# Kernel tuning notes

Hardware: AMD Instinct MI355X
Metric: run time of the kernel (lower is better)

The kernel has to match this reference:

```python
import jax, jax.numpy as jnp
import numpy as np

NUM_INSTANCES = 64  # instance ids in [0, 64); id 0 is background and excluded


def _variance_smooth_loss(variances, ins_labels, num_segments):
    # variances: [N, D] float, ins_labels: [N] int
    N, D = variances.shape
    ones = jnp.ones((N,), dtype=variances.dtype)
    counts = jax.ops.segment_sum(ones, ins_labels, num_segments=num_segments)          # [S]
    sums = jax.ops.segment_sum(variances, ins_labels, num_segments=num_segments)       # [S, D]
    safe_counts = jnp.maximum(counts, 1.0)
    means = sums / safe_counts[:, None]                                                # per-instance mean [S, D]
    diff = variances - means[ins_labels]                                               # gather means back [N, D]
    sq = jnp.sum(diff * diff, axis=1)                                                  # [N]
    # per-instance MSE = sum of squared diffs / (K_i * D), matching nn.MSELoss (mean reduction)
    per_ins = jax.ops.segment_sum(sq, ins_labels, num_segments=num_segments) / (safe_counts * D)
    valid = (counts > 0) & (jnp.arange(num_segments) != 0)                             # skip id 0 & absent ids
    return jnp.sum(jnp.where(valid, per_ins, jnp.zeros_like(per_ins)))


def setup_inputs() -> dict:
    key = jax.random.key(0)
    k1, k2 = jax.random.split(key)
    N, D = 4_000_000, 8
    variances = jax.random.normal(k1, (N, D), dtype=jnp.float32)
    ins_labels = jax.random.randint(k2, (N,), 0, NUM_INSTANCES, dtype=jnp.int32)
    return {"variances": variances, "ins_labels": ins_labels}


def reference(variances, ins_labels):
    return _variance_smooth_loss(variances, ins_labels, NUM_INSTANCES)
```

## Files before the change

### kernel.cpp

```cpp
#include <hip/hip_runtime.h>

#define NUM_INST 64
#define BLOCK 256
#define NWAVES 4
#define GRID 2048

typedef float f32x4 __attribute__((ext_vector_type(4)));
typedef short s16x8 __attribute__((ext_vector_type(8)));
typedef int   i32x4 __attribute__((ext_vector_type(4)));

union FragU { i32x4 i; s16x8 s; };

__device__ __forceinline__ unsigned hilo_pack(float v) {
    unsigned h, p;
    asm("v_cvt_pk_bf16_f32 %0, %1, %1" : "=v"(h) : "v"(v));
    const float r = v - __uint_as_float(h << 16);
    asm("v_cvt_pk_bf16_f32 %0, %1, %2" : "=v"(p) : "v"(v), "v"(r));
    return p;
}

__global__ __launch_bounds__(BLOCK) void vsl_main(const float* __restrict__ rows,
                                                  const int* __restrict__ labels,
                                                  float* __restrict__ gacc, int n) {
    const int tid = threadIdx.x;
    const int w = tid >> 6;
    const int lane = tid & 63;
    const int g = lane >> 4;
    const int c = lane & 15;
    const int cc = c & 7;

    f32x4 accS[4], accQ[4];
#pragma unroll
    for (int t = 0; t < 4; ++t) { accS[t] = (f32x4){0,0,0,0}; accQ[t] = (f32x4){0,0,0,0}; }

    const int waveId = blockIdx.x * NWAVES + w;
    const int nWavesTot = GRID * NWAVES;
    const int nChunks = (n + 15) >> 4;

    for (int ch = waveId; ch < nChunks; ch += nWavesTot) {
        const int base = ch << 4;
        const int r0 = base + 2 * g;
        unsigned b1[4], b2[4];
        int lbl[4];

        if (base + 16 <= n) {
            const int2 lp = *(const int2*)(labels + r0);
            const int2 lq = *(const int2*)(labels + r0 + 8);
            lbl[0] = lp.x; lbl[1] = lp.y; lbl[2] = lq.x; lbl[3] = lq.y;
            const float v0 = rows[(r0    ) * 8 + cc];
            const float v1 = rows[(r0 + 1) * 8 + cc];
            const float v2 = rows[(r0 + 8) * 8 + cc];
            const float v3 = rows[(r0 + 9) * 8 + cc];
            if (c < 8) {
                b1[0] = hilo_pack(v0);      b1[1] = hilo_pack(v1);
                b1[2] = hilo_pack(v2);      b1[3] = hilo_pack(v3);
                b2[0] = hilo_pack(v0 * v0); b2[1] = hilo_pack(v1 * v1);
                b2[2] = hilo_pack(v2 * v2); b2[3] = hilo_pack(v3 * v3);
            } else {
                const unsigned one = (c == 8) ? 0x3F80u : 0u;
                b1[0] = b1[1] = b1[2] = b1[3] = one;
                b2[0] = b2[1] = b2[2] = b2[3] = 0u;
            }
        } else {
#pragma unroll
            for (int q = 0; q < 4; ++q) {
                const int rq = r0 + (q & 1) + ((q >> 1) * 8);
                const bool ok = rq < n;
                const int sq = ok ? rq : 0;
                const float vq = rows[sq * 8 + cc];
                lbl[q] = ok ? labels[sq] : -1;
                if (c < 8) {
                    b1[q] = ok ? hilo_pack(vq) : 0u;
                    b2[q] = ok ? hilo_pack(vq * vq) : 0u;
                } else {
                    b1[q] = (c == 8 && ok) ? 0x3F80u : 0u;
                    b2[q] = 0u;
                }
            }
        }

        FragU B1, B2;
        B1.i = (i32x4){(int)b1[0], (int)b1[1], (int)b1[2], (int)b1[3]};
        B2.i = (i32x4){(int)b2[0], (int)b2[1], (int)b2[2], (int)b2[3]};

#pragma unroll
        for (int t = 0; t < 4; ++t) {
            const int m = c + 16 * t;
            FragU A;
            A.i = (i32x4){ lbl[0] == m ? (int)0x3F803F80 : 0,
                           lbl[1] == m ? (int)0x3F803F80 : 0,
                           lbl[2] == m ? (int)0x3F803F80 : 0,
                           lbl[3] == m ? (int)0x3F803F80 : 0 };
            accS[t] = __builtin_amdgcn_mfma_f32_16x16x32_bf16(A.s, B1.s, accS[t], 0, 0, 0);
            accQ[t] = __builtin_amdgcn_mfma_f32_16x16x32_bf16(A.s, B2.s, accQ[t], 0, 0, 0);
        }
    }

    __shared__ float red[NWAVES][NUM_INST][12];
#pragma unroll
    for (int t = 0; t < 4; ++t) {
#pragma unroll
        for (int rg = 0; rg < 4; ++rg) {
            const int Lr = 16 * t + 4 * g + rg;
            const float vS = accS[t][rg];
            if (c < 10) red[w][Lr][(c < 8) ? c : (c == 8 ? 9 : 11)] = vS;
            float sq = accQ[t][rg];
            sq += __shfl_xor(sq, 1, 64);
            sq += __shfl_xor(sq, 2, 64);
            sq += __shfl_xor(sq, 4, 64);
            if (c == 0) red[w][Lr][8] = sq;
        }
    }
    __syncthreads();

    for (int j = tid; j < NUM_INST * 10; j += BLOCK) {
        const int Lb = j / 10;
        const int st = j - Lb * 10;
        float v = 0;
#pragma unroll
        for (int ww = 0; ww < NWAVES; ++ww) v += red[ww][Lb][st];
        atomicAdd(&gacc[j], v);
    }
}

__global__ __launch_bounds__(64) void vsl_final(const float* __restrict__ gacc,
                                                float* __restrict__ out) {
    const int s = threadIdx.x;
    float val = 0.0f;
    const float* base = &gacc[s * 10];
    const float cnt = base[9];
    if (s != 0 && cnt > 0.0f) {
        const float ss = base[8];
        float m2 = 0.0f;
#pragma unroll
        for (int d = 0; d < 8; ++d) {
            const float sd = base[d];
            m2 += sd * sd;
        }
        val = (ss - m2 / cnt) / (cnt * 8.0f);
    }
#pragma unroll
    for (int off = 32; off > 0; off >>= 1) val += __shfl_down(val, off, 64);
    if (s == 0) out[0] = val;
}

extern "C" void kernel_launch(void* const* d_in, const int* in_sizes, int n_in,
                              void* d_out, int out_size, void* d_ws, size_t ws_size,
                              hipStream_t stream) {
    const float* variances = (const float*)d_in[0];
    const int* labels = (const int*)d_in[1];
    const int n = in_sizes[1];
    float* gacc = (float*)d_ws;

    hipMemsetAsync(d_ws, 0, NUM_INST * 10 * sizeof(float), stream);
    vsl_main<<<GRID, BLOCK, 0, stream>>>(variances, labels, gacc, n);
    vsl_final<<<1, 64, 0, stream>>>(gacc, (float*)d_out);
}
```

Baseline: 241.3 us.

## Stage 64-row superchunks through LDS with register prefetch of next chunk

```diff
diff --git a/kernel.cpp b/kernel.cpp
--- a/kernel.cpp
+++ b/kernel.cpp
@@ -19,9 +19,37 @@
     return p;
 }
 
+__device__ __forceinline__ void chunk_mfma(const int* lbl, float v0, float v1,
+                                           float v2, float v3, int c,
+                                           f32x4* accS, f32x4* accQ) {
+    FragU B1, B2;
+    if (c < 8) {
+        B1.i = (i32x4){(int)hilo_pack(v0), (int)hilo_pack(v1),
+                       (int)hilo_pack(v2), (int)hilo_pack(v3)};
+        B2.i = (i32x4){(int)hilo_pack(v0 * v0), (int)hilo_pack(v1 * v1),
+                       (int)hilo_pack(v2 * v2), (int)hilo_pack(v3 * v3)};
+    } else {
+        const int one = (c == 8) ? 0x3F80 : 0;
+        B1.i = (i32x4){one, one, one, one};
+        B2.i = (i32x4){0, 0, 0, 0};
+    }
+#pragma unroll
+    for (int t = 0; t < 4; ++t) {
+        const int m = c + 16 * t;
+        FragU A;
+        A.i = (i32x4){ lbl[0] == m ? (int)0x3F803F80 : 0,
+                       lbl[1] == m ? (int)0x3F803F80 : 0,
+                       lbl[2] == m ? (int)0x3F803F80 : 0,
+                       lbl[3] == m ? (int)0x3F803F80 : 0 };
+        accS[t] = __builtin_amdgcn_mfma_f32_16x16x32_bf16(A.s, B1.s, accS[t], 0, 0, 0);
+        accQ[t] = __builtin_amdgcn_mfma_f32_16x16x32_bf16(A.s, B2.s, accQ[t], 0, 0, 0);
+    }
+}
+
 __global__ __launch_bounds__(BLOCK) void vsl_main(const float* __restrict__ rows,
                                                   const int* __restrict__ labels,
                                                   float* __restrict__ gacc, int n) {
+    __shared__ float sm[3072];
     const int tid = threadIdx.x;
     const int w = tid >> 6;
     const int lane = tid & 63;
@@ -29,86 +57,96 @@
     const int c = lane & 15;
     const int cc = c & 7;
 
+    float* const wrow = sm + w * 576;
+    int* const wlab = (int*)(wrow + 512);
+
     f32x4 accS[4], accQ[4];
 #pragma unroll
     for (int t = 0; t < 4; ++t) { accS[t] = (f32x4){0,0,0,0}; accQ[t] = (f32x4){0,0,0,0}; }
 
     const int waveId = blockIdx.x * NWAVES + w;
-    const int nWavesTot = GRID * NWAVES;
-    const int nChunks = (n + 15) >> 4;
+    const int step = GRID * NWAVES;
+    const int nSC = (n + 63) >> 6;
+    const int nFullSC = n >> 6;
 
-    for (int ch = waveId; ch < nChunks; ch += nWavesTot) {
-        const int base = ch << 4;
-        const int r0 = base + 2 * g;
-        unsigned b1[4], b2[4];
-        int lbl[4];
+    f32x4 pr0 = {0,0,0,0}, pr1 = {0,0,0,0};
+    int pl = 0;
+    int sc = waveId;
+    bool stCur = (sc < nFullSC);
+    if (stCur) {
+        const float* src = rows + (size_t)sc * 512;
+        pr0 = *(const f32x4*)(src + lane * 4);
+        pr1 = *(const f32x4*)(src + 256 + lane * 4);
+        pl = labels[sc * 64 + lane];
+    }
 
-        if (base + 16 <= n) {
-            const int2 lp = *(const int2*)(labels + r0);
-            const int2 lq = *(const int2*)(labels + r0 + 8);
-            lbl[0] = lp.x; lbl[1] = lp.y; lbl[2] = lq.x; lbl[3] = lq.y;
-            const float v0 = rows[(r0    ) * 8 + cc];
-            const float v1 = rows[(r0 + 1) * 8 + cc];
-            const float v2 = rows[(r0 + 8) * 8 + cc];
-            const float v3 = rows[(r0 + 9) * 8 + cc];
-            if (c < 8) {
-                b1[0] = hilo_pack(v0);      b1[1] = hilo_pack(v1);
-                b1[2] = hilo_pack(v2);      b1[3] = hilo_pack(v3);
-                b2[0] = hilo_pack(v0 * v0); b2[1] = hilo_pack(v1 * v1);
-                b2[2] = hilo_pack(v2 * v2); b2[3] = hilo_pack(v3 * v3);
-            } else {
-                const unsigned one = (c == 8) ? 0x3F80u : 0u;
-                b1[0] = b1[1] = b1[2] = b1[3] = one;
-                b2[0] = b2[1] = b2[2] = b2[3] = 0u;
+    for (; sc < nSC; sc += step) {
+        const int scn = sc + step;
+        const bool stNext = (scn < nFullSC);
+
+        if (stCur) {
+            *(f32x4*)(wrow + lane * 4) = pr0;
+            *(f32x4*)(wrow + 256 + lane * 4) = pr1;
+            wlab[lane] = pl;
+        }
+        f32x4 nr0 = {0,0,0,0}, nr1 = {0,0,0,0};
+        int nl = 0;
+        if (stNext) {
+            const float* src = rows + (size_t)scn * 512;
+            nr0 = *(const f32x4*)(src + lane * 4);
+            nr1 = *(const f32x4*)(src + 256 + lane * 4);
+            nl = labels[scn * 64 + lane];
+        }
+
+        if (stCur) {
+#pragma unroll
+            for (int ck = 0; ck < 4; ++ck) {
+                const float* rc = wrow + ck * 128;
+                const int* lc = wlab + ck * 16;
+                const int2 lp = *(const int2*)(lc + 2 * g);
+                const int2 lq = *(const int2*)(lc + 2 * g + 8);
+                const int lbl[4] = {lp.x, lp.y, lq.x, lq.y};
+                const float v0 = rc[g * 16 + cc];
+                const float v1 = rc[g * 16 + 8 + cc];
+                const float v2 = rc[g * 16 + 64 + cc];
+                const float v3 = rc[g * 16 + 72 + cc];
+                chunk_mfma(lbl, v0, v1, v2, v3, c, accS, accQ);
             }
         } else {
+            const int base = sc << 6;
 #pragma unroll
-            for (int q = 0; q < 4; ++q) {
-                const int rq = r0 + (q & 1) + ((q >> 1) * 8);
-                const bool ok = rq < n;
-                const int sq = ok ? rq : 0;
-                const float vq = rows[sq * 8 + cc];
-                lbl[q] = ok ? labels[sq] : -1;
-                if (c < 8) {
-                    b1[q] = ok ? hilo_pack(vq) : 0u;
-                    b2[q] = ok ? hilo_pack(vq * vq) : 0u;
-                } else {
-                    b1[q] = (c == 8 && ok) ? 0x3F80u : 0u;
-                    b2[q] = 0u;
+            for (int ck = 0; ck < 4; ++ck) {
+                const int r0 = base + ck * 16 + 2 * g;
+                int lbl[4];
+                float v[4];
+#pragma unroll
+                for (int q = 0; q < 4; ++q) {
+                    const int rq = r0 + (q & 1) + ((q >> 1) << 3);
+                    const bool ok = rq < n;
+                    const int rs = ok ? rq : 0;
+                    v[q] = rows[(size_t)rs * 8 + cc];
+                    lbl[q] = ok ? labels[rs] : -1;
                 }
+                chunk_mfma(lbl, v[0], v[1], v[2], v[3], c, accS, accQ);
             }
         }
-
-        FragU B1, B2;
-        B1.i = (i32x4){(int)b1[0], (int)b1[1], (int)b1[2], (int)b1[3]};
-        B2.i = (i32x4){(int)b2[0], (int)b2[1], (int)b2[2], (int)b2[3]};
-
-#pragma unroll
-        for (int t = 0; t < 4; ++t) {
-            const int m = c + 16 * t;
-            FragU A;
-            A.i = (i32x4){ lbl[0] == m ? (int)0x3F803F80 : 0,
-                           lbl[1] == m ? (int)0x3F803F80 : 0,
-                           lbl[2] == m ? (int)0x3F803F80 : 0,
-                           lbl[3] == m ? (int)0x3F803F80 : 0 };
-            accS[t] = __builtin_amdgcn_mfma_f32_16x16x32_bf16(A.s, B1.s, accS[t], 0, 0, 0);
-            accQ[t] = __builtin_amdgcn_mfma_f32_16x16x32_bf16(A.s, B2.s, accQ[t], 0, 0, 0);
-        }
+        pr0 = nr0; pr1 = nr1; pl = nl; stCur = stNext;
     }
 
-    __shared__ float red[NWAVES][NUM_INST][12];
+    __syncthreads();
+    float* const red = sm;
 #pragma unroll
     for (int t = 0; t < 4; ++t) {
 #pragma unroll
         for (int rg = 0; rg < 4; ++rg) {
             const int Lr = 16 * t + 4 * g + rg;
             const float vS = accS[t][rg];
-            if (c < 10) red[w][Lr][(c < 8) ? c : (c == 8 ? 9 : 11)] = vS;
+            if (c < 10) red[(w * 64 + Lr) * 12 + ((c < 8) ? c : (c == 8 ? 9 : 11))] = vS;
             float sq = accQ[t][rg];
             sq += __shfl_xor(sq, 1, 64);
             sq += __shfl_xor(sq, 2, 64);
             sq += __shfl_xor(sq, 4, 64);
-            if (c == 0) red[w][Lr][8] = sq;
+            if (c == 0) red[(w * 64 + Lr) * 12 + 8] = sq;
         }
     }
     __syncthreads();
@@ -118,7 +156,7 @@
         const int st = j - Lb * 10;
         float v = 0;
 #pragma unroll
-        for (int ww = 0; ww < NWAVES; ++ww) v += red[ww][Lb][st];
+        for (int ww = 0; ww < NWAVES; ++ww) v += red[(ww * 64 + Lb) * 12 + st];
         atomicAdd(&gacc[j], v);
     }
 }
```

Measured after the change: 222.7 us. 7.7% less time.
